# Performance work log

Measured on AMD Instinct MI355X. Metric: run time of the kernel, lower is better.

Reference implementation:

```python
import jax, jax.numpy as jnp
import numpy as np
import math

H = 8
D_MODEL = 512
SEQ = 1024  # afr_reduced_cnn_size -> becomes sequence/channel axis
B = 16
KSIZE = 7
D_K = D_MODEL // H


def setup_inputs() -> dict:
    key = jax.random.key(0)
    ks = jax.random.split(key, 9)
    s = 0.02
    return {
        "query": jax.random.normal(ks[0], (B, SEQ, D_MODEL), jnp.float32),
        "key": jax.random.normal(ks[1], (B, SEQ, D_MODEL), jnp.float32),
        "value": jax.random.normal(ks[2], (B, SEQ, D_MODEL), jnp.float32),
        # causal conv params for K and V projections (convs[1], convs[2]); convs[0] is unused in forward
        "conv_k_w": jax.random.normal(ks[3], (SEQ, SEQ, KSIZE), jnp.float32) * s,
        "conv_k_b": jnp.zeros((SEQ,), jnp.float32),
        "conv_v_w": jax.random.normal(ks[4], (SEQ, SEQ, KSIZE), jnp.float32) * s,
        "conv_v_b": jnp.zeros((SEQ,), jnp.float32),
        # output linear (torch Linear: weight [out, in])
        "lin_w": jax.random.normal(ks[5], (D_MODEL, D_MODEL), jnp.float32) * s,
        "lin_b": jnp.zeros((D_MODEL,), jnp.float32),
    }


def _causal_conv1d(x, w, b):
    # x: [B, C, L]; w: [O, I, K]; left-pad K-1 for causality
    pad = w.shape[-1] - 1
    y = jax.lax.conv_general_dilated(
        x, w, window_strides=(1,), padding=[(pad, 0)],
        dimension_numbers=("NCH", "OIH", "NCH"))
    return y + b[None, :, None]


def reference(query, key, value, conv_k_w, conv_k_b, conv_v_w, conv_v_b, lin_w, lin_b):
    nb = query.shape[0]
    # [B, S, d_model] -> [B, h, N, d_k]
    q = query.reshape(nb, -1, H, D_K).transpose(0, 2, 1, 3)
    k = _causal_conv1d(key, conv_k_w, conv_k_b).reshape(nb, -1, H, D_K).transpose(0, 2, 1, 3)
    v = _causal_conv1d(value, conv_v_w, conv_v_b).reshape(nb, -1, H, D_K).transpose(0, 2, 1, 3)
    scores = jnp.einsum("bhnd,bhmd->bhnm", q, k) / math.sqrt(D_K)
    p_attn = jax.nn.softmax(scores, axis=-1)  # dropout is identity at eval
    x = jnp.einsum("bhnm,bhmd->bhnd", p_attn, v)
    x = x.transpose(0, 2, 1, 3).reshape(nb, -1, H * D_K)
    return x @ lin_w.T + lin_b
```

## Files before the change

kernel.cpp:

```cpp
#include <hip/hip_runtime.h>
#include <hip/hip_bf16.h>

typedef unsigned short u16;
typedef __attribute__((ext_vector_type(8))) __bf16 bf16x8;
typedef __attribute__((ext_vector_type(4))) float f32x4;
typedef __attribute__((ext_vector_type(4))) unsigned short u16x4;

#define DEVI static __device__ __forceinline__

DEVI u16 f2bf(float f) {
    union { float f; unsigned u; } v; v.f = f;
    unsigned r = v.u + 0x7fffu + ((v.u >> 16) & 1u);
    return (u16)(r >> 16);
}

DEVI unsigned cvt_pk_bf16(float lo, float hi) {
    unsigned r;
    asm("v_cvt_pk_bf16_f32 %0, %1, %2" : "=v"(r) : "v"(lo), "v"(hi));
    return r;
}

DEVI void gload16(const u16* g, u16* l) {
    __builtin_amdgcn_global_load_lds(
        (const __attribute__((address_space(1))) void*)g,
        (__attribute__((address_space(3))) void*)l, 16, 0, 0);
}


__global__ void k_cast_scale(const float* __restrict__ src, u16* __restrict__ dst,
                             int n, float scale) {
    int i = (blockIdx.x * blockDim.x + threadIdx.x) * 4;
    if (i >= n) return;
    float4 v = *(const float4*)(src + i);
    u16x4 o = { f2bf(v.x * scale), f2bf(v.y * scale), f2bf(v.z * scale), f2bf(v.w * scale) };
    *(u16x4*)(dst + i) = o;
}

__global__ void k_castW(const float* __restrict__ w, u16* __restrict__ wt) {
    int oi = blockIdx.x * blockDim.x + threadIdx.x;
    const float* p = w + (size_t)oi * 7;
#pragma unroll
    for (int t = 0; t < 7; ++t)
        wt[(size_t)t * 1048576 + oi] = f2bf(p[t]);
}

__global__ void k_transpose_pad(const float* __restrict__ x, u16* __restrict__ out) {
    __shared__ float tile[64][65];
    int b = blockIdx.z;
    int l0 = blockIdx.x * 64, i0 = blockIdx.y * 64;
    int t = threadIdx.x;
    const float* xb = x + (size_t)b * 1024 * 512;
    u16* ob = out + (size_t)b * 520 * 1024;
    if (blockIdx.x == 0 && t < 96) {
        int pr = t >> 4, pc = (t & 15) * 4;
        u16x4 z = { 0, 0, 0, 0 };
        *(u16x4*)(ob + (size_t)pr * 1024 + i0 + pc) = z;
    }
    int tr = t >> 4, tc = (t & 15) * 4;
#pragma unroll
    for (int r = 0; r < 4; ++r) {
        int row = tr + r * 16;
        float4 v = *(const float4*)(xb + (size_t)(i0 + row) * 512 + l0 + tc);
        tile[row][tc + 0] = v.x; tile[row][tc + 1] = v.y;
        tile[row][tc + 2] = v.z; tile[row][tc + 3] = v.w;
    }
    __syncthreads();
#pragma unroll
    for (int r = 0; r < 4; ++r) {
        int lr = tr + r * 16;
        u16x4 o = { f2bf(tile[tc + 0][lr]), f2bf(tile[tc + 1][lr]),
                    f2bf(tile[tc + 2][lr]), f2bf(tile[tc + 3][lr]) };
        *(u16x4*)(ob + (size_t)(l0 + 6 + lr) * 1024 + i0 + tc) = o;
    }
}

__global__ __launch_bounds__(512, 2)
void k_conv256(const u16* __restrict__ WtK, const u16* __restrict__ WtV,
               const u16* __restrict__ XtK, const u16* __restrict__ XtV,
               const float* __restrict__ bK, const float* __restrict__ bV,
               u16* __restrict__ YK, u16* __restrict__ YV) {
    __shared__ __align__(16) u16 As[2][16384];
    __shared__ __align__(16) u16 Bs[2][16896];
    int id = blockIdx.x;
    int xcd = id & 7, inner = id >> 3;
    bool isV = xcd & 1;
    int o0 = (xcd >> 1) * 256;
    int b = inner & 15;
    int l0 = (inner >> 4) * 256;
    const u16* Wt = isV ? WtV : WtK;
    const u16* Xb = (isV ? XtV : XtK) + (size_t)b * 520 * 1024;
    int tid = threadIdx.x, lane = tid & 63, wave = tid >> 6;
    int q = lane & 15, g = lane >> 4;
    int wm = wave >> 2, wn = wave & 3;

    int sr = tid >> 3;
    int ss = (tid & 7) ^ (sr & 7);

    auto stageA = [&](int ic, int t, int slot) {
        const u16* a = Wt + ((size_t)t << 20) + (size_t)(o0 + sr) * 1024 + (ic << 6) + ss * 8;
        u16* ad = &As[slot][tid * 8];
#pragma unroll
        for (int l = 0; l < 4; ++l)
            gload16(a + (size_t)(l << 6) * 1024, ad + (l << 12));
    };
    auto stageB = [&](int ic, int slot) {
        const u16* bb = Xb + (size_t)(l0 + sr) * 1024 + (ic << 6) + ss * 8;
        u16* bd = &Bs[slot][tid * 8];
#pragma unroll
        for (int l = 0; l < 4; ++l)
            gload16(bb + (size_t)(l << 6) * 1024, bd + (l << 12));
        int sr5 = 256 + ((tid >> 3) & 7);
        gload16(Xb + (size_t)(l0 + sr5) * 1024 + (ic << 6) + ss * 8,
                &Bs[slot][sr5 * 64 + (tid & 7) * 8]);
    };

    f32x4 acc[8][4] = {};

    stageB(0, 0);
    stageA(0, 0, 0);
    stageA(0, 1, 1);
    asm volatile("s_waitcnt vmcnt(4)" ::: "memory");
    __builtin_amdgcn_s_barrier();

    int ic2 = 0, t2 = 2;
    for (int ic = 0; ic < 16; ++ic) {
        int bslot = ic & 1;
        const u16* Bsl = Bs[bslot];
        for (int t = 0; t < 7; ++t) {
            int s = ic * 7 + t;
            const u16* Asl = As[s & 1];
            bf16x8 bfr[4][2], af[4][2];
#pragma unroll
            for (int nf = 0; nf < 4; ++nf) {
                int r = wn * 64 + nf * 16 + q + t;
                const u16* base = Bsl + r * 64;
#pragma unroll
                for (int kk = 0; kk < 2; ++kk)
                    bfr[nf][kk] = *(const bf16x8*)(base + (((kk * 4 + g) ^ (r & 7)) << 3));
            }
#pragma unroll
            for (int mf = 0; mf < 4; ++mf) {
                int r = wm * 128 + mf * 16 + q;
                const u16* base = Asl + r * 64;
#pragma unroll
                for (int kk = 0; kk < 2; ++kk)
                    af[mf][kk] = *(const bf16x8*)(base + (((kk * 4 + g) ^ (r & 7)) << 3));
            }
#pragma unroll
            for (int mf = 0; mf < 4; ++mf)
#pragma unroll
                for (int nf = 0; nf < 4; ++nf)
#pragma unroll
                    for (int kk = 0; kk < 2; ++kk)
                        acc[mf][nf] = __builtin_amdgcn_mfma_f32_16x16x32_bf16(
                            af[mf][kk], bfr[nf][kk], acc[mf][nf], 0, 0, 0);
#pragma unroll
            for (int mf = 0; mf < 4; ++mf) {
                int r = wm * 128 + 64 + mf * 16 + q;
                const u16* base = Asl + r * 64;
#pragma unroll
                for (int kk = 0; kk < 2; ++kk)
                    af[mf][kk] = *(const bf16x8*)(base + (((kk * 4 + g) ^ (r & 7)) << 3));
            }
#pragma unroll
            for (int mf = 0; mf < 4; ++mf)
#pragma unroll
                for (int nf = 0; nf < 4; ++nf)
#pragma unroll
                    for (int kk = 0; kk < 2; ++kk)
                        acc[4 + mf][nf] = __builtin_amdgcn_mfma_f32_16x16x32_bf16(
                            af[mf][kk], bfr[nf][kk], acc[4 + mf][nf], 0, 0, 0);

            asm volatile("" ::: "memory");
            __builtin_amdgcn_s_barrier();
            bool haveB = (t == 2) && (ic < 15);
            if (s + 2 < 112) {
                stageA(ic2, t2, s & 1);
                if (++t2 == 7) { t2 = 0; ++ic2; }
                if (haveB) stageB(ic + 1, bslot ^ 1);
                if (haveB || (t == 3 && ic < 15))
                    asm volatile("s_waitcnt vmcnt(9)" ::: "memory");
                else
                    asm volatile("s_waitcnt vmcnt(4)" ::: "memory");
            } else {
                asm volatile("s_waitcnt vmcnt(0)" ::: "memory");
            }
            __builtin_amdgcn_s_barrier();
        }
    }

    const float* bias = isV ? bV : bK;
#pragma unroll
    for (int mf = 0; mf < 8; ++mf) {
        int ro = o0 + wm * 128 + mf * 16 + g * 4;
        float b0 = bias[ro + 0], b1 = bias[ro + 1], b2 = bias[ro + 2], b3 = bias[ro + 3];
#pragma unroll
        for (int nf = 0; nf < 4; ++nf) {
            int co = l0 + wn * 64 + nf * 16 + q;
            f32x4 a = acc[mf][nf];
            if (isV) {
                u16x4 o = { f2bf(a[0] + b0), f2bf(a[1] + b1), f2bf(a[2] + b2), f2bf(a[3] + b3) };
                *(u16x4*)&YV[((size_t)b * 512 + co) * 1024 + ro] = o;
            } else {
                u16* yp = &YK[((size_t)b * 1024 + ro) * 512 + co];
                yp[0]    = f2bf(a[0] + b0);
                yp[512]  = f2bf(a[1] + b1);
                yp[1024] = f2bf(a[2] + b2);
                yp[1536] = f2bf(a[3] + b3);
            }
        }
    }
}

__global__ __launch_bounds__(512, 4)
void k_attn2(const u16* __restrict__ Q, const u16* __restrict__ K,
             const u16* __restrict__ Vt, u16* __restrict__ O) {
    __shared__ __align__(16) u16 Ks[2][64 * 64];
    __shared__ __align__(16) u16 Vs[2][64 * 64];
    int b = blockIdx.z, h = blockIdx.y, q0 = blockIdx.x * 128;
    int tid = threadIdx.x, lane = tid & 63, wave = tid >> 6;
    int g = lane >> 4, q = lane & 15;

    const u16* Kb = K + (size_t)b * 1024 * 512 + h * 64;
    const u16* Vb = Vt + ((size_t)b * 512 + h * 64) * 1024;
    const u16* Qb = Q + ((size_t)b * 1024 + q0 + wave * 16 + q) * 512 + h * 64;

    bf16x8 qf[2];
    qf[0] = *(const bf16x8*)(Qb + g * 8);
    qf[1] = *(const bf16x8*)(Qb + 32 + g * 8);

    int sr = tid >> 3;
    int ss = (tid & 7) ^ (sr & 7);
    const u16* ksrc = Kb + (size_t)sr * 512 + ss * 8;
    const u16* vsrc = Vb + (size_t)sr * 1024 + ss * 8;

    f32x4 o[4] = {};
    float lsum = 0.f;

    gload16(ksrc, &Ks[0][tid * 8]);
    gload16(vsrc, &Vs[0][tid * 8]);
    __syncthreads();

#pragma unroll 2
    for (int t = 0; t < 16; ++t) {
        int buf = t & 1;
        if (t < 15) {
            gload16(ksrc + (size_t)(t + 1) * 64 * 512, &Ks[buf ^ 1][tid * 8]);
            gload16(vsrc + (t + 1) * 64, &Vs[buf ^ 1][tid * 8]);
        }
        f32x4 s[4];
#pragma unroll
        for (int mf = 0; mf < 4; ++mf) {
            int r = 16 * mf + q;
            const u16* base = &Ks[buf][r * 64];
            bf16x8 kf0 = *(const bf16x8*)(base + (((g) ^ (q & 7)) << 3));
            bf16x8 kf1 = *(const bf16x8*)(base + (((4 + g) ^ (q & 7)) << 3));
            f32x4 zz = {};
            zz = __builtin_amdgcn_mfma_f32_16x16x32_bf16(kf0, qf[0], zz, 0, 0, 0);
            s[mf] = __builtin_amdgcn_mfma_f32_16x16x32_bf16(kf1, qf[1], zz, 0, 0, 0);
        }
        unsigned w[4][2];
#pragma unroll
        for (int mf = 0; mf < 4; ++mf) {
            f32x4 p;
#pragma unroll
            for (int j = 0; j < 4; ++j) {
                p[j] = exp2f(s[mf][j]);
                lsum += p[j];
            }
            w[mf][0] = cvt_pk_bf16(p[0], p[1]);
            w[mf][1] = cvt_pk_bf16(p[2], p[3]);
        }
        bool hi = lane >= 32;
        int ia = ((g & 1) << 5) + q;
        int ib = ia + 16;
#pragma unroll
        for (int c = 0; c < 2; ++c) {
            unsigned a0 = __shfl(w[2 * c][0], ia), b0 = __shfl(w[2 * c + 1][0], ia);
            unsigned a1 = __shfl(w[2 * c][1], ia), b1 = __shfl(w[2 * c + 1][1], ia);
            unsigned a2 = __shfl(w[2 * c][0], ib), b2 = __shfl(w[2 * c + 1][0], ib);
            unsigned a3 = __shfl(w[2 * c][1], ib), b3 = __shfl(w[2 * c + 1][1], ib);
            union { unsigned u[4]; bf16x8 v8; } pu;
            pu.u[0] = hi ? b0 : a0;
            pu.u[1] = hi ? b1 : a1;
            pu.u[2] = hi ? b2 : a2;
            pu.u[3] = hi ? b3 : a3;
            bf16x8 pb = pu.v8;
#pragma unroll
            for (int df = 0; df < 4; ++df) {
                int rd = 16 * df + q;
                bf16x8 vf = *(const bf16x8*)(&Vs[buf][rd * 64] + (((c * 4 + g) ^ (q & 7)) << 3));
                o[df] = __builtin_amdgcn_mfma_f32_16x16x32_bf16(vf, pb, o[df], 0, 0, 0);
            }
        }
        __syncthreads();
    }

    lsum += __shfl_xor(lsum, 16);
    lsum += __shfl_xor(lsum, 32);
    float inv = 1.0f / lsum;

    unsigned wo[4][2];
#pragma unroll
    for (int df = 0; df < 4; ++df) {
        f32x4 v = o[df];
        v[0] *= inv; v[1] *= inv; v[2] *= inv; v[3] *= inv;
        wo[df][0] = cvt_pk_bf16(v[0], v[1]);
        wo[df][1] = cvt_pk_bf16(v[2], v[3]);
    }
    bool hi = lane >= 32;
    int ia = ((g & 1) << 5) + q;
    int ib = ia + 16;
    u16* Ob = O + ((size_t)b * 1024 + q0 + wave * 16 + q) * 512 + h * 64;
#pragma unroll
    for (int c = 0; c < 2; ++c) {
        unsigned a0 = __shfl(wo[2 * c][0], ia), b0 = __shfl(wo[2 * c + 1][0], ia);
        unsigned a1 = __shfl(wo[2 * c][1], ia), b1 = __shfl(wo[2 * c + 1][1], ia);
        unsigned a2 = __shfl(wo[2 * c][0], ib), b2 = __shfl(wo[2 * c + 1][0], ib);
        unsigned a3 = __shfl(wo[2 * c][1], ib), b3 = __shfl(wo[2 * c + 1][1], ib);
        int4 st;
        st.x = (int)(hi ? b0 : a0);
        st.y = (int)(hi ? b1 : a1);
        st.z = (int)(hi ? b2 : a2);
        st.w = (int)(hi ? b3 : a3);
        *(int4*)(Ob + c * 32 + g * 8) = st;
    }
}

__global__ __launch_bounds__(256, 2)
void k_gemm_out(const u16* __restrict__ A, const u16* __restrict__ Bt,
                const float* __restrict__ bias, float* __restrict__ C) {
    __shared__ __align__(16) u16 As[128 * 64];
    __shared__ __align__(16) u16 Bs[128 * 64];
    int n0 = blockIdx.x * 128, m0 = blockIdx.y * 128;
    int tid = threadIdx.x, lane = tid & 63, wave = tid >> 6;
    int wr = (wave >> 1) * 64, wc = (wave & 1) * 64;
    f32x4 acc[4][4] = {};

    for (int kk = 0; kk < 8; ++kk) {
        int i0 = kk * 64;
        const u16* asrc = A + (size_t)(m0 + (tid >> 3)) * 512 + i0 + (tid & 7) * 8;
        const u16* bsrc = Bt + (size_t)(n0 + (tid >> 3)) * 512 + i0 + (tid & 7) * 8;
        __syncthreads();
#pragma unroll
        for (int s = 0; s < 4; ++s) {
            gload16(asrc + (size_t)s * 32 * 512, &As[s * 2048 + tid * 8]);
            gload16(bsrc + (size_t)s * 32 * 512, &Bs[s * 2048 + tid * 8]);
        }
        __syncthreads();
#pragma unroll
        for (int ks = 0; ks < 2; ++ks) {
            bf16x8 af[4], bfr[4];
#pragma unroll
            for (int m = 0; m < 4; ++m)
                af[m] = *(const bf16x8*)&As[(wr + m * 16 + (lane & 15)) * 64 + ks * 32 + (lane >> 4) * 8];
#pragma unroll
            for (int n = 0; n < 4; ++n)
                bfr[n] = *(const bf16x8*)&Bs[(wc + n * 16 + (lane & 15)) * 64 + ks * 32 + (lane >> 4) * 8];
#pragma unroll
            for (int m = 0; m < 4; ++m)
#pragma unroll
                for (int n = 0; n < 4; ++n)
                    acc[m][n] = __builtin_amdgcn_mfma_f32_16x16x32_bf16(af[m], bfr[n], acc[m][n], 0, 0, 0);
        }
    }

#pragma unroll
    for (int m = 0; m < 4; ++m) {
        int ro = m0 + wr + m * 16 + (lane >> 4) * 4;
#pragma unroll
        for (int n = 0; n < 4; ++n) {
            int co = n0 + wc + n * 16 + (lane & 15);
            float bb = bias[co];
            float* cp = &C[(size_t)ro * 512 + co];
            cp[0]    = acc[m][n][0] + bb;
            cp[512]  = acc[m][n][1] + bb;
            cp[1024] = acc[m][n][2] + bb;
            cp[1536] = acc[m][n][3] + bb;
        }
    }
}

extern "C" void kernel_launch(void* const* d_in, const int* in_sizes, int n_in,
                              void* d_out, int out_size, void* d_ws, size_t ws_size,
                              hipStream_t stream) {
    (void)in_sizes; (void)n_in; (void)out_size; (void)ws_size;
    const float* query = (const float*)d_in[0];
    const float* key   = (const float*)d_in[1];
    const float* value = (const float*)d_in[2];
    const float* wk    = (const float*)d_in[3];
    const float* bk    = (const float*)d_in[4];
    const float* wv    = (const float*)d_in[5];
    const float* bv    = (const float*)d_in[6];
    const float* lw    = (const float*)d_in[7];
    const float* lb    = (const float*)d_in[8];
    float* out = (float*)d_out;

    u16* ws16  = (u16*)d_ws;
    u16* q_bf  = ws16;
    u16* k_att = q_bf  + 8388608;
    u16* v_t   = k_att + 8388608;
    u16* x_att = v_t   + 8388608;
    u16* xt_k  = x_att + 8388608;
    u16* xt_v  = xt_k  + 8519680;
    u16* wk_bf = xt_v  + 8519680;
    u16* wv_bf = wk_bf + 7340032;
    u16* lw_bf = wv_bf + 7340032;

    k_cast_scale<<<8192, 256, 0, stream>>>(query, q_bf, 8388608, 0.125f * 1.44269504f);
    k_cast_scale<<<256, 256, 0, stream>>>(lw, lw_bf, 262144, 1.0f);
    k_castW<<<4096, 256, 0, stream>>>(wk, wk_bf);
    k_castW<<<4096, 256, 0, stream>>>(wv, wv_bf);
    k_transpose_pad<<<dim3(8, 16, 16), 256, 0, stream>>>(key, xt_k);
    k_transpose_pad<<<dim3(8, 16, 16), 256, 0, stream>>>(value, xt_v);

    k_conv256<<<dim3(256, 1, 1), 512, 0, stream>>>(wk_bf, wv_bf, xt_k, xt_v, bk, bv, k_att, v_t);

    k_attn2<<<dim3(8, 8, 16), 512, 0, stream>>>(q_bf, k_att, v_t, x_att);

    k_gemm_out<<<dim3(4, 128), 256, 0, stream>>>(x_att, lw_bf, lb, out);
}
```

Before: 338.0 us.

## Shrink causal-conv GEMM tile to 128 outputs with 256-thread blocks

Replaces the 256x256-tile, 512-thread conv kernel with a 128x256-tile, 256-thread kernel launched on 512 blocks. The aim is more blocks per CU and better latency hiding on the conv GEMM. The input (B) tile drops from double to single buffering and is now loaded after the barrier at the last tap of each chunk, with a single uniform waitcnt. In exchange, each block reuses less data per load, and the B load for each new chunk is no longer overlapped with compute.

Measured after the change: 323.3 us. 1.05x faster.

```diff
diff --git a/kernel.cpp b/kernel.cpp
--- a/kernel.cpp
+++ b/kernel.cpp
@@ -74,24 +74,24 @@
     }
 }
 
-__global__ __launch_bounds__(512, 2)
-void k_conv256(const u16* __restrict__ WtK, const u16* __restrict__ WtV,
+__global__ __launch_bounds__(256, 2)
+void k_conv128(const u16* __restrict__ WtK, const u16* __restrict__ WtV,
                const u16* __restrict__ XtK, const u16* __restrict__ XtV,
                const float* __restrict__ bK, const float* __restrict__ bV,
                u16* __restrict__ YK, u16* __restrict__ YV) {
-    __shared__ __align__(16) u16 As[2][16384];
-    __shared__ __align__(16) u16 Bs[2][16896];
+    __shared__ __align__(16) u16 As[2][8192];
+    __shared__ __align__(16) u16 Bs[16896];
     int id = blockIdx.x;
-    int xcd = id & 7, inner = id >> 3;
-    bool isV = xcd & 1;
-    int o0 = (xcd >> 1) * 256;
+    int o0 = (id & 7) * 128;
+    bool isV = (id >> 3) & 1;
+    int inner = id >> 4;
     int b = inner & 15;
     int l0 = (inner >> 4) * 256;
     const u16* Wt = isV ? WtV : WtK;
     const u16* Xb = (isV ? XtV : XtK) + (size_t)b * 520 * 1024;
     int tid = threadIdx.x, lane = tid & 63, wave = tid >> 6;
     int q = lane & 15, g = lane >> 4;
-    int wm = wave >> 2, wn = wave & 3;
+    int wm = wave >> 1, wn = wave & 1;
 
     int sr = tid >> 3;
     int ss = (tid & 7) ^ (sr & 7);
@@ -101,22 +101,22 @@
         u16* ad = &As[slot][tid * 8];
 #pragma unroll
         for (int l = 0; l < 4; ++l)
-            gload16(a + (size_t)(l << 6) * 1024, ad + (l << 12));
+            gload16(a + (size_t)(l << 5) * 1024, ad + (l << 11));
     };
-    auto stageB = [&](int ic, int slot) {
+    auto stageB = [&](int ic) {
         const u16* bb = Xb + (size_t)(l0 + sr) * 1024 + (ic << 6) + ss * 8;
-        u16* bd = &Bs[slot][tid * 8];
-#pragma unroll
-        for (int l = 0; l < 4; ++l)
-            gload16(bb + (size_t)(l << 6) * 1024, bd + (l << 12));
-        int sr5 = 256 + ((tid >> 3) & 7);
+        u16* bd = &Bs[tid * 8];
+#pragma unroll
+        for (int l = 0; l < 8; ++l)
+            gload16(bb + (size_t)(l << 5) * 1024, bd + (l << 11));
+        int sr5 = 256 + (sr & 7);
         gload16(Xb + (size_t)(l0 + sr5) * 1024 + (ic << 6) + ss * 8,
-                &Bs[slot][sr5 * 64 + (tid & 7) * 8]);
+                &Bs[sr5 * 64 + (tid & 7) * 8]);
     };
 
-    f32x4 acc[8][4] = {};
-
-    stageB(0, 0);
+    f32x4 acc[4][8] = {};
+
+    stageB(0);
     stageA(0, 0, 0);
     stageA(0, 1, 1);
     asm volatile("s_waitcnt vmcnt(4)" ::: "memory");
@@ -124,27 +124,26 @@
 
     int ic2 = 0, t2 = 2;
     for (int ic = 0; ic < 16; ++ic) {
-        int bslot = ic & 1;
-        const u16* Bsl = Bs[bslot];
         for (int t = 0; t < 7; ++t) {
             int s = ic * 7 + t;
             const u16* Asl = As[s & 1];
-            bf16x8 bfr[4][2], af[4][2];
+            bf16x8 af[4][2], bfr[4][2];
+
+#pragma unroll
+            for (int mf = 0; mf < 4; ++mf) {
+                int r = wm * 64 + mf * 16 + q;
+                const u16* base = Asl + r * 64;
+#pragma unroll
+                for (int kk = 0; kk < 2; ++kk)
+                    af[mf][kk] = *(const bf16x8*)(base + (((kk * 4 + g) ^ (r & 7)) << 3));
+            }
 #pragma unroll
             for (int nf = 0; nf < 4; ++nf) {
-                int r = wn * 64 + nf * 16 + q + t;
-                const u16* base = Bsl + r * 64;
+                int r = wn * 128 + nf * 16 + q + t;
+                const u16* base = Bs + r * 64;
 #pragma unroll
                 for (int kk = 0; kk < 2; ++kk)
                     bfr[nf][kk] = *(const bf16x8*)(base + (((kk * 4 + g) ^ (r & 7)) << 3));
-            }
-#pragma unroll
-            for (int mf = 0; mf < 4; ++mf) {
-                int r = wm * 128 + mf * 16 + q;
-                const u16* base = Asl + r * 64;
-#pragma unroll
-                for (int kk = 0; kk < 2; ++kk)
-                    af[mf][kk] = *(const bf16x8*)(base + (((kk * 4 + g) ^ (r & 7)) << 3));
             }
 #pragma unroll
             for (int mf = 0; mf < 4; ++mf)
@@ -154,13 +153,14 @@
                     for (int kk = 0; kk < 2; ++kk)
                         acc[mf][nf] = __builtin_amdgcn_mfma_f32_16x16x32_bf16(
                             af[mf][kk], bfr[nf][kk], acc[mf][nf], 0, 0, 0);
-#pragma unroll
-            for (int mf = 0; mf < 4; ++mf) {
-                int r = wm * 128 + 64 + mf * 16 + q;
-                const u16* base = Asl + r * 64;
+
+#pragma unroll
+            for (int nf = 0; nf < 4; ++nf) {
+                int r = wn * 128 + (4 + nf) * 16 + q + t;
+                const u16* base = Bs + r * 64;
 #pragma unroll
                 for (int kk = 0; kk < 2; ++kk)
-                    af[mf][kk] = *(const bf16x8*)(base + (((kk * 4 + g) ^ (r & 7)) << 3));
+                    bfr[nf][kk] = *(const bf16x8*)(base + (((kk * 4 + g) ^ (r & 7)) << 3));
             }
 #pragma unroll
             for (int mf = 0; mf < 4; ++mf)
@@ -168,20 +168,16 @@
                 for (int nf = 0; nf < 4; ++nf)
 #pragma unroll
                     for (int kk = 0; kk < 2; ++kk)
-                        acc[4 + mf][nf] = __builtin_amdgcn_mfma_f32_16x16x32_bf16(
-                            af[mf][kk], bfr[nf][kk], acc[4 + mf][nf], 0, 0, 0);
+                        acc[mf][4 + nf] = __builtin_amdgcn_mfma_f32_16x16x32_bf16(
+                            af[mf][kk], bfr[nf][kk], acc[mf][4 + nf], 0, 0, 0);
 
             asm volatile("" ::: "memory");
             __builtin_amdgcn_s_barrier();
-            bool haveB = (t == 2) && (ic < 15);
             if (s + 2 < 112) {
+                if (t == 6) stageB(ic + 1);
                 stageA(ic2, t2, s & 1);
                 if (++t2 == 7) { t2 = 0; ++ic2; }
-                if (haveB) stageB(ic + 1, bslot ^ 1);
-                if (haveB || (t == 3 && ic < 15))
-                    asm volatile("s_waitcnt vmcnt(9)" ::: "memory");
-                else
-                    asm volatile("s_waitcnt vmcnt(4)" ::: "memory");
+                asm volatile("s_waitcnt vmcnt(4)" ::: "memory");
             } else {
                 asm volatile("s_waitcnt vmcnt(0)" ::: "memory");
             }
@@ -191,12 +187,12 @@
 
     const float* bias = isV ? bV : bK;
 #pragma unroll
-    for (int mf = 0; mf < 8; ++mf) {
-        int ro = o0 + wm * 128 + mf * 16 + g * 4;
+    for (int mf = 0; mf < 4; ++mf) {
+        int ro = o0 + wm * 64 + mf * 16 + g * 4;
         float b0 = bias[ro + 0], b1 = bias[ro + 1], b2 = bias[ro + 2], b3 = bias[ro + 3];
 #pragma unroll
-        for (int nf = 0; nf < 4; ++nf) {
-            int co = l0 + wn * 64 + nf * 16 + q;
+        for (int nf = 0; nf < 8; ++nf) {
+            int co = l0 + wn * 128 + nf * 16 + q;
             f32x4 a = acc[mf][nf];
             if (isV) {
                 u16x4 o = { f2bf(a[0] + b0), f2bf(a[1] + b1), f2bf(a[2] + b2), f2bf(a[3] + b3) };
@@ -414,7 +410,7 @@
     k_transpose_pad<<<dim3(8, 16, 16), 256, 0, stream>>>(key, xt_k);
     k_transpose_pad<<<dim3(8, 16, 16), 256, 0, stream>>>(value, xt_v);
 
-    k_conv256<<<dim3(256, 1, 1), 512, 0, stream>>>(wk_bf, wv_bf, xt_k, xt_v, bk, bv, k_att, v_t);
+    k_conv128<<<dim3(512, 1, 1), 256, 0, stream>>>(wk_bf, wv_bf, xt_k, xt_v, bk, bv, k_att, v_t);
 
     k_attn2<<<dim3(8, 8, 16), 512, 0, stream>>>(q_bf, k_att, v_t, x_att);
 
```
